# Kernel optimization log

Hardware: AMD Instinct MI355X
Metric: run time of the kernel (lower is better)

The kernel has to match this reference:

```python
import jax, jax.numpy as jnp
import numpy as np
import itertools

GRID = 256          # voxel grid extent per axis (coords in [0, GRID))
KSIZE = 3           # kernel_size
OFFSETS = np.array(list(itertools.product(range(KSIZE), repeat=3)), dtype=np.int32) - (KSIZE // 2)  # [27,3]


def setup_inputs() -> dict:
    key = jax.random.key(0)
    k1, k2, k3 = jax.random.split(key, 3)
    N, Cin, Cout = 262144, 64, 64
    coords = jax.random.randint(k1, (N, 3), 0, GRID, dtype=jnp.int32)
    feats = jax.random.normal(k2, (N, Cin), dtype=jnp.float32)
    kernel = jax.random.normal(k3, (KSIZE ** 3, Cin, Cout), dtype=jnp.float32) * 0.02
    return {"coords": coords, "feats": feats, "kernel": kernel}


def reference(coords, feats, kernel):
    # Submanifold sparse conv3d: out[i] = sum_k feats[j_k(i)] @ kernel[k]
    # where coords[j_k(i)] == coords[i] + offset_k (if such a point exists).
    N = coords.shape[0]
    Cout = kernel.shape[-1]
    # Hash table: linearized voxel -> point index (-1 if empty).
    lin = (coords[:, 0] * GRID + coords[:, 1]) * GRID + coords[:, 2]
    table = jnp.full((GRID ** 3,), -1, dtype=jnp.int32).at[lin].set(
        jnp.arange(N, dtype=jnp.int32))
    out = jnp.zeros((N, Cout), dtype=feats.dtype)
    for k in range(KSIZE ** 3):
        off = jnp.asarray(OFFSETS[k])              # [3]
        nc = coords + off[None, :]                 # neighbor coords [N,3]
        in_bounds = jnp.all((nc >= 0) & (nc < GRID), axis=1)
        nlin = (nc[:, 0] * GRID + nc[:, 1]) * GRID + nc[:, 2]
        idx = table[jnp.clip(nlin, 0, GRID ** 3 - 1)]
        valid = in_bounds & (idx >= 0)
        g = feats[jnp.where(valid, idx, 0)] * valid[:, None].astype(feats.dtype)  # [N,Cin]
        out = out + g @ kernel[k]                  # [N,Cout]
    return out
```

## Files before the change

kernel.cpp:

```cpp
#include <hip/hip_runtime.h>

#define VGRID 256
#define N_TAPS 27
#define CIN 64
#define COUT 64
#define PAIR_CAP 16384
#define CNT_STRIDE 16
#define LCAP 64

typedef short short8 __attribute__((ext_vector_type(8)));
typedef float float4v __attribute__((ext_vector_type(4)));

__device__ __forceinline__ short f2bf(float x) {
    unsigned u = __builtin_bit_cast(unsigned, x);
    unsigned r = (u + 0x7FFF + ((u >> 16) & 1)) >> 16;
    return (short)r;
}

__global__ void __launch_bounds__(256) build_kernel(
        const int* __restrict__ coords, int* __restrict__ table,
        unsigned* __restrict__ bits, const float* __restrict__ W,
        short* __restrict__ Wt, int n, int bt_blocks) {
    if ((int)blockIdx.x >= bt_blocks) {
        int tap = blockIdx.x - bt_blocks;
        for (int e = threadIdx.x; e < CIN * COUT; e += 256) {
            int ci = e >> 6, co = e & 63;
            Wt[((size_t)tap * COUT + co) * CIN + ci] =
                f2bf(W[((size_t)tap * CIN + ci) * COUT + co]);
        }
        return;
    }
    int i = blockIdx.x * 256 + threadIdx.x;
    if (i >= n) return;
    int lin = (coords[i * 3 + 0] * VGRID + coords[i * 3 + 1]) * VGRID + coords[i * 3 + 2];
    atomicMax(&table[lin], i);
    atomicOr(&bits[lin >> 5], 1u << (lin & 31));
}

__global__ void __launch_bounds__(256) probe_center_kernel(
        const int* __restrict__ coords, const int* __restrict__ table,
        const unsigned* __restrict__ bits,
        int* __restrict__ counters, int2* __restrict__ pairs,
        const float* __restrict__ feats, const short* __restrict__ Wt,
        float* __restrict__ out, int n) {
    __shared__ int lcnt[26];
    __shared__ int lbase[26];
    __shared__ int2 lpairs[26][LCAP];
    __shared__ int jc_s[256];
    __shared__ short a_lds[64][CIN + 8];

    int t = threadIdx.x;
    int i = blockIdx.x * 256 + t;
    if (t < 26) lcnt[t] = 0;
    __syncthreads();

    int cx = 0, cy = 0, cz = 0;
    unsigned hitmask = 0;
    int center_idx = 0;
    if (i < n) {
        cx = coords[i * 3 + 0];
        cy = coords[i * 3 + 1];
        cz = coords[i * 3 + 2];
        int clin = (cx * VGRID + cy) * VGRID + cz;
        center_idx = table[clin];

        unsigned w[N_TAPS];
#pragma unroll
        for (int k = 0; k < N_TAPS; ++k) {
            int ox = k / 9 - 1, oy = (k / 3) % 3 - 1, oz = k % 3 - 1;
            int nx = cx + ox, ny = cy + oy, nz = cz + oz;
            bool v = ((unsigned)nx < VGRID) && ((unsigned)ny < VGRID) &&
                     ((unsigned)nz < VGRID);
            int nlin = (nx * VGRID + ny) * VGRID + nz;
            w[k] = v ? bits[(unsigned)nlin >> 5] : 0u;
        }
#pragma unroll
        for (int k = 0; k < N_TAPS; ++k) {
            if (k == 13) continue;
            int nz = cz + (k % 3 - 1);
            if ((w[k] >> (nz & 31)) & 1u) hitmask |= 1u << k;
        }
    }
    jc_s[t] = center_idx;

    while (__builtin_amdgcn_ballot_w64(hitmask != 0)) {
        if (hitmask) {
            int k = __builtin_ctz(hitmask);
            hitmask &= hitmask - 1;
            int ox = k / 9 - 1, oy = (k / 3) % 3 - 1, oz = k % 3 - 1;
            int nlin = ((cx + ox) * VGRID + (cy + oy)) * VGRID + (cz + oz);
            int idx = table[nlin];
            int kidx = k - (k > 13);
            int pos = atomicAdd(&lcnt[kidx], 1);
            if (pos < LCAP) lpairs[kidx][pos] = make_int2(i, idx);
        }
    }
    __syncthreads();

    if (t < 26) {
        int c = lcnt[t];
        if (c > LCAP) c = LCAP;
        lcnt[t] = c;
        lbase[t] = atomicAdd(&counters[t * CNT_STRIDE], c);
    }
    __syncthreads();

    int wave = t >> 6, lane = t & 63;
    for (int k = wave; k < 26; k += 4) {
        int c = lcnt[k];
        if (lane < c) {
            int pos = lbase[k] + lane;
            if (pos < PAIR_CAP) pairs[(size_t)k * PAIR_CAP + pos] = lpairs[k][lane];
        }
    }

    int quad = lane >> 4, m = lane & 15;
    const short* W13 = Wt + 13 * CIN * COUT;
    int base = blockIdx.x * 256;

    for (int rt = 0; rt < 4; ++rt) {
        __syncthreads();
        {
            int r = t >> 2;
            int seg = (t & 3) * 16;
            int grow = base + rt * 64 + r;
            int j = (grow < n) ? jc_s[rt * 64 + r] : 0;
            const float4* src = (const float4*)(feats + (size_t)j * CIN + seg);
#pragma unroll
            for (int q = 0; q < 4; ++q) {
                float4 v = src[q];
                a_lds[r][seg + q * 4 + 0] = f2bf(v.x);
                a_lds[r][seg + q * 4 + 1] = f2bf(v.y);
                a_lds[r][seg + q * 4 + 2] = f2bf(v.z);
                a_lds[r][seg + q * 4 + 3] = f2bf(v.w);
            }
        }
        __syncthreads();

        int row0 = wave * 16;
#pragma unroll
        for (int nt = 0; nt < 4; ++nt) {
            float4v acc = {0.f, 0.f, 0.f, 0.f};
            int nn = nt * 16 + m;
#pragma unroll
            for (int ks = 0; ks < 2; ++ks) {
                short8 a = *(const short8*)&a_lds[row0 + m][ks * 32 + quad * 8];
                short8 b = *(const short8*)(W13 + (size_t)nn * CIN + ks * 32 + quad * 8);
                acc = __builtin_amdgcn_mfma_f32_16x16x32_bf16(a, b, acc, 0, 0, 0);
            }
#pragma unroll
            for (int r2 = 0; r2 < 4; ++r2) {
                int orow = base + rt * 64 + row0 + quad * 4 + r2;
                if (orow < n) out[(size_t)orow * COUT + nn] = acc[r2];
            }
        }
    }
}

__global__ void __launch_bounds__(256) scatter_gemm_kernel(
        const float* __restrict__ feats, const short* __restrict__ Wt,
        const int* __restrict__ counters, const int2* __restrict__ pairs,
        float* __restrict__ out) {
    __shared__ short a_lds[64][CIN + 8];
    __shared__ int i_arr[64];

    int kidx = blockIdx.y;
    int tap = kidx + (kidx >= 13);
    int cnt = counters[kidx * CNT_STRIDE];
    if (cnt > PAIR_CAP) cnt = PAIR_CAP;
    int ntiles = (cnt + 63) >> 6;
    const short* W = Wt + (size_t)tap * CIN * COUT;
    const int2* P = pairs + (size_t)kidx * PAIR_CAP;

    int t = threadIdx.x;
    int wave = t >> 6, lane = t & 63;
    int quad = lane >> 4, m = lane & 15;

    for (int tile = blockIdx.x; tile < ntiles; tile += gridDim.x) {
        int tbase = tile * 64;
        int rem = cnt - tbase;
        if (rem > 64) rem = 64;

        if (t < 64) i_arr[t] = (t < rem) ? P[tbase + t].x : -1;
        {
            int r = t >> 2;
            int seg = (t & 3) * 16;
            int j = (r < rem) ? P[tbase + r].y : -1;
#pragma unroll
            for (int q = 0; q < 4; ++q) {
                float4 v = {0.f, 0.f, 0.f, 0.f};
                if (j >= 0) v = *(const float4*)(feats + (size_t)j * CIN + seg + q * 4);
                a_lds[r][seg + q * 4 + 0] = f2bf(v.x);
                a_lds[r][seg + q * 4 + 1] = f2bf(v.y);
                a_lds[r][seg + q * 4 + 2] = f2bf(v.z);
                a_lds[r][seg + q * 4 + 3] = f2bf(v.w);
            }
        }
        __syncthreads();

        int row0 = wave * 16;
#pragma unroll
        for (int nt = 0; nt < 4; ++nt) {
            float4v acc = {0.f, 0.f, 0.f, 0.f};
            int nn = nt * 16 + m;
#pragma unroll
            for (int ks = 0; ks < 2; ++ks) {
                short8 a = *(const short8*)&a_lds[row0 + m][ks * 32 + quad * 8];
                short8 b = *(const short8*)(W + (size_t)nn * CIN + ks * 32 + quad * 8);
                acc = __builtin_amdgcn_mfma_f32_16x16x32_bf16(a, b, acc, 0, 0, 0);
            }
#pragma unroll
            for (int r2 = 0; r2 < 4; ++r2) {
                int i = i_arr[row0 + quad * 4 + r2];
                if (i >= 0) atomicAdd(&out[(size_t)i * COUT + nn], acc[r2]);
            }
        }
        __syncthreads();
    }
}

extern "C" void kernel_launch(void* const* d_in, const int* in_sizes, int n_in,
                              void* d_out, int out_size, void* d_ws, size_t ws_size,
                              hipStream_t stream) {
    const int* coords = (const int*)d_in[0];
    const float* feats = (const float*)d_in[1];
    const float* weights = (const float*)d_in[2];
    float* out = (float*)d_out;

    int n = in_sizes[0] / 3;

    char* ws = (char*)d_ws;
    size_t BITMAP_BYTES = (size_t)VGRID * VGRID * VGRID / 8;
    unsigned* bits = (unsigned*)ws;
    int* counters = (int*)(ws + BITMAP_BYTES);
    short* wbft = (short*)(ws + BITMAP_BYTES + 4096);
    int2* pairs = (int2*)(ws + BITMAP_BYTES + 4096 + 221184);
    int* table = (int*)(ws + BITMAP_BYTES + 4096 + 221184
                        + (size_t)26 * PAIR_CAP * 8);

    hipMemsetAsync(ws, 0, BITMAP_BYTES + 4096, stream);

    int bt_blocks = (n + 255) / 256;
    build_kernel<<<bt_blocks + N_TAPS, 256, 0, stream>>>(coords, table, bits,
                                                         weights, wbft, n, bt_blocks);

    probe_center_kernel<<<bt_blocks, 256, 0, stream>>>(coords, table, bits,
                                                       counters, pairs, feats,
                                                       wbft, out, n);

    dim3 sg_grid(96, 26);
    scatter_gemm_kernel<<<sg_grid, 256, 0, stream>>>(feats, wbft, counters, pairs, out);
}
```

Before: 215.0 us.

## Fuse neighbor probing and per-tap GEMM into one gather-based kernel

Replaces the pair-list build plus separate scatter-GEMM with atomics by one kernel. Each wave gathers neighbor features for its 16-row groups and accumulates every active tap's MFMA in registers before a plain store. Weights are repacked so each lane's B fragment is one contiguous short8 load, and bitmap probing now reads 2 words per xy-row instead of 27. This removes the pair buffers, the counters, the per-tap atomic accumulation and the earlier LCAP/PAIR_CAP caps that could drop pairs. In exchange, it runs MFMAs over the union of taps present in each 16-row group, with zero-filled rows for points that lack a neighbor.

```diff
diff --git a/kernel.cpp b/kernel.cpp
--- a/kernel.cpp
+++ b/kernel.cpp
@@ -4,9 +4,6 @@
 #define N_TAPS 27
 #define CIN 64
 #define COUT 64
-#define PAIR_CAP 16384
-#define CNT_STRIDE 16
-#define LCAP 64
 
 typedef short short8 __attribute__((ext_vector_type(8)));
 typedef float float4v __attribute__((ext_vector_type(4)));
@@ -25,7 +22,8 @@
         int tap = blockIdx.x - bt_blocks;
         for (int e = threadIdx.x; e < CIN * COUT; e += 256) {
             int ci = e >> 6, co = e & 63;
-            Wt[((size_t)tap * COUT + co) * CIN + ci] =
+            int ks = ci >> 5, quad = (ci >> 3) & 3, el = ci & 7;
+            Wt[((((size_t)tap * 2 + ks) * 4 + quad) * 64 + co) * 8 + el] =
                 f2bf(W[((size_t)tap * CIN + ci) * COUT + co]);
         }
         return;
@@ -37,22 +35,14 @@
     atomicOr(&bits[lin >> 5], 1u << (lin & 31));
 }
 
-__global__ void __launch_bounds__(256) probe_center_kernel(
+__global__ void __launch_bounds__(256) fused_kernel(
         const int* __restrict__ coords, const int* __restrict__ table,
-        const unsigned* __restrict__ bits,
-        int* __restrict__ counters, int2* __restrict__ pairs,
-        const float* __restrict__ feats, const short* __restrict__ Wt,
-        float* __restrict__ out, int n) {
-    __shared__ int lcnt[26];
-    __shared__ int lbase[26];
-    __shared__ int2 lpairs[26][LCAP];
-    __shared__ int jc_s[256];
-    __shared__ short a_lds[64][CIN + 8];
-
+        const unsigned* __restrict__ bits, const float* __restrict__ feats,
+        const short* __restrict__ Wt, float* __restrict__ out, int n) {
     int t = threadIdx.x;
+    int lane = t & 63;
     int i = blockIdx.x * 256 + t;
-    if (t < 26) lcnt[t] = 0;
-    __syncthreads();
+    int wbase = blockIdx.x * 256 + (t & 192);
 
     int cx = 0, cy = 0, cz = 0;
     unsigned hitmask = 0;
@@ -64,158 +54,129 @@
         int clin = (cx * VGRID + cy) * VGRID + cz;
         center_idx = table[clin];
 
-        unsigned w[N_TAPS];
-#pragma unroll
-        for (int k = 0; k < N_TAPS; ++k) {
-            int ox = k / 9 - 1, oy = (k / 3) % 3 - 1, oz = k % 3 - 1;
-            int nx = cx + ox, ny = cy + oy, nz = cz + oz;
-            bool v = ((unsigned)nx < VGRID) && ((unsigned)ny < VGRID) &&
-                     ((unsigned)nz < VGRID);
-            int nlin = (nx * VGRID + ny) * VGRID + nz;
-            w[k] = v ? bits[(unsigned)nlin >> 5] : 0u;
+        int zlo = cz > 0 ? cz - 1 : 0;
+        int zhi = cz < VGRID - 1 ? cz + 1 : VGRID - 1;
+        int wlo = zlo >> 5, whi = zhi >> 5;
+        unsigned rw0[9], rw1[9];
+#pragma unroll
+        for (int r = 0; r < 9; ++r) {
+            int nx = cx + r / 3 - 1, ny = cy + r % 3 - 1;
+            bool v = ((unsigned)nx < VGRID) && ((unsigned)ny < VGRID);
+            int rb = ((nx * VGRID + ny) * VGRID) >> 5;
+            rw0[r] = v ? bits[rb + wlo] : 0u;
+            rw1[r] = v ? bits[rb + whi] : 0u;
         }
 #pragma unroll
         for (int k = 0; k < N_TAPS; ++k) {
             if (k == 13) continue;
-            int nz = cz + (k % 3 - 1);
-            if ((w[k] >> (nz & 31)) & 1u) hitmask |= 1u << k;
-        }
-    }
-    jc_s[t] = center_idx;
-
-    while (__builtin_amdgcn_ballot_w64(hitmask != 0)) {
-        if (hitmask) {
-            int k = __builtin_ctz(hitmask);
-            hitmask &= hitmask - 1;
-            int ox = k / 9 - 1, oy = (k / 3) % 3 - 1, oz = k % 3 - 1;
-            int nlin = ((cx + ox) * VGRID + (cy + oy)) * VGRID + (cz + oz);
-            int idx = table[nlin];
-            int kidx = k - (k > 13);
-            int pos = atomicAdd(&lcnt[kidx], 1);
-            if (pos < LCAP) lpairs[kidx][pos] = make_int2(i, idx);
-        }
-    }
-    __syncthreads();
-
-    if (t < 26) {
-        int c = lcnt[t];
-        if (c > LCAP) c = LCAP;
-        lcnt[t] = c;
-        lbase[t] = atomicAdd(&counters[t * CNT_STRIDE], c);
-    }
-    __syncthreads();
-
-    int wave = t >> 6, lane = t & 63;
-    for (int k = wave; k < 26; k += 4) {
-        int c = lcnt[k];
-        if (lane < c) {
-            int pos = lbase[k] + lane;
-            if (pos < PAIR_CAP) pairs[(size_t)k * PAIR_CAP + pos] = lpairs[k][lane];
-        }
-    }
-
-    int quad = lane >> 4, m = lane & 15;
-    const short* W13 = Wt + 13 * CIN * COUT;
-    int base = blockIdx.x * 256;
-
-    for (int rt = 0; rt < 4; ++rt) {
-        __syncthreads();
+            int nz = cz + k % 3 - 1;
+            if ((unsigned)nz < VGRID) {
+                unsigned wrd = ((nz >> 5) == wlo) ? rw0[k / 3] : rw1[k / 3];
+                hitmask |= ((wrd >> (nz & 31)) & 1u) << k;
+            }
+        }
+    }
+
+    int p0 = 0, p1 = 0, p2 = 0, p3 = 0;
+    {
+        unsigned hm = hitmask;
+        int cnt = 0;
+        while (hm) {
+            int k = __builtin_ctz(hm); hm &= hm - 1u;
+            int nlin = ((cx + k / 9 - 1) * VGRID + (cy + (k / 3) % 3 - 1)) * VGRID
+                       + (cz + k % 3 - 1);
+            int j = table[nlin];
+            if (cnt == 0) p0 = j; else if (cnt == 1) p1 = j;
+            else if (cnt == 2) p2 = j; else if (cnt == 3) p3 = j;
+            ++cnt;
+        }
+    }
+
+    int packed = (cx << 16) | (cy << 8) | cz;
+
+    unsigned gmor = hitmask;
+    gmor |= (unsigned)__shfl_xor((int)gmor, 1);
+    gmor |= (unsigned)__shfl_xor((int)gmor, 2);
+    gmor |= (unsigned)__shfl_xor((int)gmor, 4);
+    gmor |= (unsigned)__shfl_xor((int)gmor, 8);
+
+    int m = lane & 15, quad = lane >> 4;
+    const short8* Bp = (const short8*)Wt;
+
+    for (int g = 0; g < 4; ++g) {
+        int src = g * 16 + m;
+        int rpk = __shfl(packed, src);
+        unsigned rhm = (unsigned)__shfl((int)hitmask, src);
+        int rjc = __shfl(center_idx, src);
+        int rp0 = __shfl(p0, src), rp1 = __shfl(p1, src);
+        int rp2 = __shfl(p2, src), rp3 = __shfl(p3, src);
+        unsigned gor = (unsigned)__shfl((int)gmor, g * 16);
+        gor = __builtin_amdgcn_readfirstlane(gor);
+
+        float4v acc[4] = {{0,0,0,0},{0,0,0,0},{0,0,0,0},{0,0,0,0}};
+
         {
-            int r = t >> 2;
-            int seg = (t & 3) * 16;
-            int grow = base + rt * 64 + r;
-            int j = (grow < n) ? jc_s[rt * 64 + r] : 0;
-            const float4* src = (const float4*)(feats + (size_t)j * CIN + seg);
-#pragma unroll
-            for (int q = 0; q < 4; ++q) {
-                float4 v = src[q];
-                a_lds[r][seg + q * 4 + 0] = f2bf(v.x);
-                a_lds[r][seg + q * 4 + 1] = f2bf(v.y);
-                a_lds[r][seg + q * 4 + 2] = f2bf(v.z);
-                a_lds[r][seg + q * 4 + 3] = f2bf(v.w);
-            }
-        }
-        __syncthreads();
-
-        int row0 = wave * 16;
-#pragma unroll
-        for (int nt = 0; nt < 4; ++nt) {
-            float4v acc = {0.f, 0.f, 0.f, 0.f};
-            int nn = nt * 16 + m;
-#pragma unroll
-            for (int ks = 0; ks < 2; ++ks) {
-                short8 a = *(const short8*)&a_lds[row0 + m][ks * 32 + quad * 8];
-                short8 b = *(const short8*)(W13 + (size_t)nn * CIN + ks * 32 + quad * 8);
-                acc = __builtin_amdgcn_mfma_f32_16x16x32_bf16(a, b, acc, 0, 0, 0);
-            }
+            const float* fr = feats + (size_t)rjc * CIN + quad * 8;
+            float4 u0 = *(const float4*)(fr);
+            float4 u1 = *(const float4*)(fr + 4);
+            float4 v0 = *(const float4*)(fr + 32);
+            float4 v1 = *(const float4*)(fr + 36);
+            short8 a0 = {f2bf(u0.x), f2bf(u0.y), f2bf(u0.z), f2bf(u0.w),
+                         f2bf(u1.x), f2bf(u1.y), f2bf(u1.z), f2bf(u1.w)};
+            short8 a1 = {f2bf(v0.x), f2bf(v0.y), f2bf(v0.z), f2bf(v0.w),
+                         f2bf(v1.x), f2bf(v1.y), f2bf(v1.z), f2bf(v1.w)};
+#pragma unroll
+            for (int nt = 0; nt < 4; ++nt) {
+                short8 b0 = Bp[((13 * 2 + 0) * 4 + quad) * 64 + nt * 16 + m];
+                short8 b1 = Bp[((13 * 2 + 1) * 4 + quad) * 64 + nt * 16 + m];
+                acc[nt] = __builtin_amdgcn_mfma_f32_16x16x32_bf16(a0, b0, acc[nt], 0, 0, 0);
+                acc[nt] = __builtin_amdgcn_mfma_f32_16x16x32_bf16(a1, b1, acc[nt], 0, 0, 0);
+            }
+        }
+
+        unsigned gm = gor;
+        while (gm) {
+            int k = (int)__builtin_ctz(gm); gm &= gm - 1u;
+            bool has = (rhm >> k) & 1u;
+            short8 h0 = {0,0,0,0,0,0,0,0}, h1 = {0,0,0,0,0,0,0,0};
+            if (has) {
+                int rank = __builtin_popcount(rhm & ((1u << k) - 1u));
+                int j2;
+                if (rank == 0) j2 = rp0;
+                else if (rank == 1) j2 = rp1;
+                else if (rank == 2) j2 = rp2;
+                else if (rank == 3) j2 = rp3;
+                else {
+                    int rx = (rpk >> 16) & 255, ry = (rpk >> 8) & 255, rz = rpk & 255;
+                    j2 = table[((rx + k / 9 - 1) * VGRID + (ry + (k / 3) % 3 - 1)) * VGRID
+                               + (rz + k % 3 - 1)];
+                }
+                const float* hr = feats + (size_t)j2 * CIN + quad * 8;
+                float4 u0 = *(const float4*)(hr);
+                float4 u1 = *(const float4*)(hr + 4);
+                float4 v0 = *(const float4*)(hr + 32);
+                float4 v1 = *(const float4*)(hr + 36);
+                h0 = (short8){f2bf(u0.x), f2bf(u0.y), f2bf(u0.z), f2bf(u0.w),
+                              f2bf(u1.x), f2bf(u1.y), f2bf(u1.z), f2bf(u1.w)};
+                h1 = (short8){f2bf(v0.x), f2bf(v0.y), f2bf(v0.z), f2bf(v0.w),
+                              f2bf(v1.x), f2bf(v1.y), f2bf(v1.z), f2bf(v1.w)};
+            }
+#pragma unroll
+            for (int nt = 0; nt < 4; ++nt) {
+                short8 b0 = Bp[((k * 2 + 0) * 4 + quad) * 64 + nt * 16 + m];
+                short8 b1 = Bp[((k * 2 + 1) * 4 + quad) * 64 + nt * 16 + m];
+                acc[nt] = __builtin_amdgcn_mfma_f32_16x16x32_bf16(h0, b0, acc[nt], 0, 0, 0);
+                acc[nt] = __builtin_amdgcn_mfma_f32_16x16x32_bf16(h1, b1, acc[nt], 0, 0, 0);
+            }
+        }
+
+#pragma unroll
+        for (int nt = 0; nt < 4; ++nt)
 #pragma unroll
             for (int r2 = 0; r2 < 4; ++r2) {
-                int orow = base + rt * 64 + row0 + quad * 4 + r2;
-                if (orow < n) out[(size_t)orow * COUT + nn] = acc[r2];
-            }
-        }
-    }
-}
-
-__global__ void __launch_bounds__(256) scatter_gemm_kernel(
-        const float* __restrict__ feats, const short* __restrict__ Wt,
-        const int* __restrict__ counters, const int2* __restrict__ pairs,
-        float* __restrict__ out) {
-    __shared__ short a_lds[64][CIN + 8];
-    __shared__ int i_arr[64];
-
-    int kidx = blockIdx.y;
-    int tap = kidx + (kidx >= 13);
-    int cnt = counters[kidx * CNT_STRIDE];
-    if (cnt > PAIR_CAP) cnt = PAIR_CAP;
-    int ntiles = (cnt + 63) >> 6;
-    const short* W = Wt + (size_t)tap * CIN * COUT;
-    const int2* P = pairs + (size_t)kidx * PAIR_CAP;
-
-    int t = threadIdx.x;
-    int wave = t >> 6, lane = t & 63;
-    int quad = lane >> 4, m = lane & 15;
-
-    for (int tile = blockIdx.x; tile < ntiles; tile += gridDim.x) {
-        int tbase = tile * 64;
-        int rem = cnt - tbase;
-        if (rem > 64) rem = 64;
-
-        if (t < 64) i_arr[t] = (t < rem) ? P[tbase + t].x : -1;
-        {
-            int r = t >> 2;
-            int seg = (t & 3) * 16;
-            int j = (r < rem) ? P[tbase + r].y : -1;
-#pragma unroll
-            for (int q = 0; q < 4; ++q) {
-                float4 v = {0.f, 0.f, 0.f, 0.f};
-                if (j >= 0) v = *(const float4*)(feats + (size_t)j * CIN + seg + q * 4);
-                a_lds[r][seg + q * 4 + 0] = f2bf(v.x);
-                a_lds[r][seg + q * 4 + 1] = f2bf(v.y);
-                a_lds[r][seg + q * 4 + 2] = f2bf(v.z);
-                a_lds[r][seg + q * 4 + 3] = f2bf(v.w);
-            }
-        }
-        __syncthreads();
-
-        int row0 = wave * 16;
-#pragma unroll
-        for (int nt = 0; nt < 4; ++nt) {
-            float4v acc = {0.f, 0.f, 0.f, 0.f};
-            int nn = nt * 16 + m;
-#pragma unroll
-            for (int ks = 0; ks < 2; ++ks) {
-                short8 a = *(const short8*)&a_lds[row0 + m][ks * 32 + quad * 8];
-                short8 b = *(const short8*)(W + (size_t)nn * CIN + ks * 32 + quad * 8);
-                acc = __builtin_amdgcn_mfma_f32_16x16x32_bf16(a, b, acc, 0, 0, 0);
-            }
-#pragma unroll
-            for (int r2 = 0; r2 < 4; ++r2) {
-                int i = i_arr[row0 + quad * 4 + r2];
-                if (i >= 0) atomicAdd(&out[(size_t)i * COUT + nn], acc[r2]);
-            }
-        }
-        __syncthreads();
+                int orow = wbase + g * 16 + quad * 4 + r2;
+                if (orow < n) out[(size_t)orow * COUT + nt * 16 + m] = acc[nt][r2];
+            }
     }
 }
 
@@ -232,22 +193,15 @@
     char* ws = (char*)d_ws;
     size_t BITMAP_BYTES = (size_t)VGRID * VGRID * VGRID / 8;
     unsigned* bits = (unsigned*)ws;
-    int* counters = (int*)(ws + BITMAP_BYTES);
-    short* wbft = (short*)(ws + BITMAP_BYTES + 4096);
-    int2* pairs = (int2*)(ws + BITMAP_BYTES + 4096 + 221184);
-    int* table = (int*)(ws + BITMAP_BYTES + 4096 + 221184
-                        + (size_t)26 * PAIR_CAP * 8);
-
-    hipMemsetAsync(ws, 0, BITMAP_BYTES + 4096, stream);
+    short* wbft = (short*)(ws + BITMAP_BYTES);
+    int* table = (int*)(ws + ((size_t)4 << 20));
+
+    hipMemsetAsync(ws, 0, BITMAP_BYTES, stream);
 
     int bt_blocks = (n + 255) / 256;
     build_kernel<<<bt_blocks + N_TAPS, 256, 0, stream>>>(coords, table, bits,
                                                          weights, wbft, n, bt_blocks);
 
-    probe_center_kernel<<<bt_blocks, 256, 0, stream>>>(coords, table, bits,
-                                                       counters, pairs, feats,
-                                                       wbft, out, n);
-
-    dim3 sg_grid(96, 26);
-    scatter_gemm_kernel<<<sg_grid, 256, 0, stream>>>(feats, wbft, counters, pairs, out);
-}
+    fused_kernel<<<bt_blocks, 256, 0, stream>>>(coords, table, bits, feats,
+                                                wbft, out, n);
+}
```

New measurement: 222.6 us. 1.04x slower.
